# Performance work log

Hardware: AMD Instinct MI355X
Metric: run time of the kernel (lower is better)

Reference implementation:

```python
import jax, jax.numpy as jnp
import numpy as np

B, WIN, NN, NF, NH, NOUT = 4, 10, 10000, 8, 64, 1
N = B * WIN * NN          # stacked graph nodes
E = 3200000               # edges
EPS = 1e-5                # BatchNorm eps


def _gcn(x, edge_index, ew, W, b):
    # PyG GCNConv: linear first, then sym-normalized aggregation with self loops.
    xl = x @ W  # [N, H]
    loop = jnp.arange(N)
    row = jnp.concatenate([edge_index[0], loop])
    col = jnp.concatenate([edge_index[1], loop])
    w = jnp.concatenate([ew, jnp.ones((N,), ew.dtype)])
    deg = jax.ops.segment_sum(w, col, num_segments=N)
    dinv = jnp.where(deg > 0, jax.lax.rsqrt(deg), 0.0)
    norm = dinv[row] * w * dinv[col]
    out = jax.ops.segment_sum(norm[:, None] * xl[row], col, num_segments=N)
    return out + b


def _bn(x, g, bta):
    # training-mode BatchNorm1d (batch statistics, biased variance)
    m = x.mean(0)
    v = x.var(0)
    return (x - m) * jax.lax.rsqrt(v + EPS) * g + bta


def _lstm(xs, wih, whh, bih, bhh):
    # xs: [T, Bn, D]; PyTorch gate order i, f, g, o
    H = whh.shape[1]
    Bn = xs.shape[1]
    h0 = jnp.zeros((Bn, H), xs.dtype)
    c0 = jnp.zeros((Bn, H), xs.dtype)
    def step(carry, xt):
        h, c = carry
        gates = xt @ wih.T + bih + h @ whh.T + bhh
        i, f, g, o = jnp.split(gates, 4, axis=-1)
        c = jax.nn.sigmoid(f) * c + jax.nn.sigmoid(i) * jnp.tanh(g)
        h = jax.nn.sigmoid(o) * jnp.tanh(c)
        return (h, c), h
    (hn, cn), ys = jax.lax.scan(step, (h0, c0), xs)
    return ys, hn


def setup_inputs() -> dict:
    key = jax.random.key(0)
    ks = jax.random.split(key, 16)
    def rn(k, shape, s=0.05):
        return jax.random.normal(k, shape, jnp.float32) * s
    return {
        "x": jax.random.normal(ks[0], (N, NF), jnp.float32),
        "edge_index": jax.random.randint(ks[1], (2, E), 0, N),
        "edge_weight": jax.random.uniform(ks[2], (E,), jnp.float32),
        "c1_w": rn(ks[3], (NF, NH)), "c1_b": jnp.zeros((NH,), jnp.float32),
        "c2_w": rn(ks[4], (NH, NH)), "c2_b": jnp.zeros((NH,), jnp.float32),
        "bn1_g": jnp.ones((NH,), jnp.float32), "bn1_b": jnp.zeros((NH,), jnp.float32),
        "bn2_g": jnp.ones((NH,), jnp.float32), "bn2_b": jnp.zeros((NH,), jnp.float32),
        "l1_wih": rn(ks[5], (4 * NH, 2 * NH)), "l1_whh": rn(ks[6], (4 * NH, NH)),
        "l1_bih": jnp.zeros((4 * NH,), jnp.float32), "l1_bhh": jnp.zeros((4 * NH,), jnp.float32),
        "l2_wih": rn(ks[7], (4 * NH, NH)), "l2_whh": rn(ks[8], (4 * NH, NH)),
        "l2_bih": jnp.zeros((4 * NH,), jnp.float32), "l2_bhh": jnp.zeros((4 * NH,), jnp.float32),
        "fc1_w": rn(ks[9], (NH, 2 * NH + WIN * NF)), "fc1_b": jnp.zeros((NH,), jnp.float32),
        "fc2_w": rn(ks[10], (NOUT, NH)), "fc2_b": jnp.zeros((NOUT,), jnp.float32),
    }


def reference(x, edge_index, edge_weight, c1_w, c1_b, c2_w, c2_b,
              bn1_g, bn1_b, bn2_g, bn2_b,
              l1_wih, l1_whh, l1_bih, l1_bhh,
              l2_wih, l2_whh, l2_bih, l2_bhh,
              fc1_w, fc1_b, fc2_w, fc2_b):
    # skip connection: raw features per (batch,node) over the window
    skip = x.reshape(B, WIN, NN, NF).transpose(0, 2, 1, 3).reshape(B * NN, WIN * NF)
    # two GCN layers (dropout is identity in deterministic/eval reference)
    h1 = _bn(jax.nn.relu(_gcn(x, edge_index, edge_weight, c1_w, c1_b)), bn1_g, bn1_b)
    h2 = _bn(jax.nn.relu(_gcn(h1, edge_index, edge_weight, c2_w, c2_b)), bn2_g, bn2_b)
    xc = jnp.concatenate([h1, h2], axis=1)  # [N, 2H]
    xr = xc.reshape(B, WIN, NN, 2 * NH).transpose(1, 0, 2, 3).reshape(WIN, B * NN, 2 * NH)
    ys1, hn1 = _lstm(xr, l1_wih, l1_whh, l1_bih, l1_bhh)
    ys2, hn2 = _lstm(ys1, l2_wih, l2_whh, l2_bih, l2_bhh)
    z = jnp.concatenate([hn1, hn2, skip], axis=1)
    z = jax.nn.relu(z @ fc1_w.T + fc1_b)
    z = jax.nn.relu(z @ fc2_w.T + fc2_b)
    return z.reshape(-1)
```

## Files before the change

kernel.cpp:

```cpp
#include <hip/hip_runtime.h>
#include <math.h>

constexpr int BB     = 4;
constexpr int WINN   = 10;
constexpr int NNODES = 10000;
constexpr int NFEAT  = 8;
constexpr int NHID   = 64;
constexpr int NTOT   = BB * WINN * NNODES;
constexpr int NEDGE  = 3200000;
constexpr int NBN    = BB * NNODES;
constexpr float EPSBN = 1e-5f;

#define DEVFN static __device__ __forceinline__

typedef float f4 __attribute__((ext_vector_type(4)));
typedef short s8v __attribute__((ext_vector_type(8)));
typedef unsigned short ushort_t;
typedef unsigned int uint_t;

DEVFN float sigmoidf_(float x) { return 1.0f / (1.0f + __expf(-x)); }
DEVFN float tanhf_(float x) { return 2.0f / (1.0f + __expf(-2.0f * x)) - 1.0f; }
DEVFN ushort_t f2bf(float f) {
    uint_t x = __float_as_uint(f);
    return (ushort_t)((x + 0x7FFFu + ((x >> 16) & 1u)) >> 16);
}
DEVFN float bf2f(ushort_t u) { return __uint_as_float(((uint_t)u) << 16); }

__global__ void k_diag(float* out, float wsz, int n) {
    int i = blockIdx.x * 256 + threadIdx.x;
    if (i < n) out[i] = wsz;
}

__global__ void k_init(int* cntP, float* sums) {
    int i = blockIdx.x * 256 + threadIdx.x;
    if (i < 8 * NTOT) cntP[i] = 0;
    if (i < 2048) sums[i] = 0.f;
}

__global__ void k_hist(const int* __restrict__ ei, int* __restrict__ cntP) {
    int e = blockIdx.x * 256 + threadIdx.x;
    int p = blockIdx.x & 7;
    if (e < NEDGE) atomicAdd(&cntP[p * NTOT + ei[NEDGE + e]], 1);
}

__global__ void k_scan1(const int* __restrict__ cntP, int* __restrict__ ptr, int* __restrict__ tmp) {
    __shared__ int sdat[256];
    int tid = threadIdx.x;
    int base = blockIdx.x * 1024 + tid * 4;
    int v[4];
#pragma unroll
    for (int j = 0; j < 4; ++j) {
        int idx = base + j;
        int s = 0;
        if (idx < NTOT) {
#pragma unroll
            for (int p = 0; p < 8; ++p) s += cntP[p * NTOT + idx];
        }
        v[j] = s;
    }
    int sum = v[0] + v[1] + v[2] + v[3];
    sdat[tid] = sum;
    __syncthreads();
    for (int ofs = 1; ofs < 256; ofs <<= 1) {
        int x = (tid >= ofs) ? sdat[tid - ofs] : 0;
        __syncthreads();
        sdat[tid] += x;
        __syncthreads();
    }
    int run = sdat[tid] - sum;
    if (base + 0 < NTOT) ptr[base + 0] = run; run += v[0];
    if (base + 1 < NTOT) ptr[base + 1] = run; run += v[1];
    if (base + 2 < NTOT) ptr[base + 2] = run; run += v[2];
    if (base + 3 < NTOT) ptr[base + 3] = run;
    if (tid == 255) tmp[blockIdx.x] = sdat[255];
}

__global__ void k_scan2(int* tmp, int nb) {
    __shared__ int st[512];
    int tid = threadIdx.x;
    int v = (tid < nb) ? tmp[tid] : 0;
    st[tid] = v;
    __syncthreads();
    for (int ofs = 1; ofs < 512; ofs <<= 1) {
        int x = (tid >= ofs) ? st[tid - ofs] : 0;
        __syncthreads();
        st[tid] += x;
        __syncthreads();
    }
    if (tid < nb) tmp[tid] = st[tid] - v;
}

__global__ void k_scan3(int* __restrict__ ptr, int* __restrict__ cntP, const int* __restrict__ tmp) {
    int i = blockIdx.x * 256 + threadIdx.x;
    if (i < NTOT) {
        int p0 = ptr[i] + tmp[i >> 10];
        ptr[i] = p0;
        int run = p0;
#pragma unroll
        for (int p = 0; p < 8; ++p) {
            int c = cntP[p * NTOT + i];
            cntP[p * NTOT + i] = run;
            run += c;
        }
    }
    if (i == 0) ptr[NTOT] = NEDGE;
}

__global__ void k_fill(const int* __restrict__ ei, const float* __restrict__ ew,
                       int* __restrict__ cur8, int2* __restrict__ epack) {
    int e = blockIdx.x * 256 + threadIdx.x;
    if (e >= NEDGE) return;
    int p = blockIdx.x & 7;
    int row = ei[e], col = ei[NEDGE + e];
    int pos = atomicAdd(&cur8[p * NTOT + col], 1);
    epack[pos] = make_int2(row, __float_as_int(ew[e]));
}

__global__ void k_degcsr(const int* __restrict__ ptr, const int2* __restrict__ epack,
                         float* __restrict__ dinv) {
    int tid = threadIdx.x;
    int lane = tid & 63;
    int waveg = blockIdx.x * 4 + (tid >> 6);
    int g = lane >> 3, sub = lane & 7;
    int node = waveg * 8 + g;
    int beg = ptr[node], end = ptr[node + 1];
    float s = 0.f;
    for (int e = beg + sub; e < end; e += 8) s += __int_as_float(epack[e].y);
    s += __shfl_xor(s, 1, 64);
    s += __shfl_xor(s, 2, 64);
    s += __shfl_xor(s, 4, 64);
    if (sub == 0) dinv[node] = rsqrtf(1.0f + s);
}

__global__ void k_gather8(const int* __restrict__ ptr, const int2* __restrict__ epack,
                          const float* __restrict__ x, const float* __restrict__ dinv,
                          float* __restrict__ aggX) {
    int tid = threadIdx.x;
    int lane = tid & 63;
    int waveg = blockIdx.x * 4 + (tid >> 6);
    int g = lane >> 3, ch = lane & 7;
    int node = waveg * 8 + g;
    int beg = ptr[node], end = ptr[node + 1];
    float dv = dinv[node];
    float accE = 0.f;
    int e = beg;
    for (; e + 1 < end; e += 2) {
        int2 p0 = epack[e], p1 = epack[e + 1];
        accE = fmaf(dinv[p0.x] * __int_as_float(p0.y), x[p0.x * 8 + ch], accE);
        accE = fmaf(dinv[p1.x] * __int_as_float(p1.y), x[p1.x * 8 + ch], accE);
    }
    if (e < end) {
        int2 p = epack[e];
        accE = fmaf(dinv[p.x] * __int_as_float(p.y), x[p.x * 8 + ch], accE);
    }
    aggX[node * 8 + ch] = dv * fmaf(dv, x[node * 8 + ch], accE);
}

__global__ void k_gather64(const int* __restrict__ ptr, const int2* __restrict__ epack,
                           const ushort_t* __restrict__ src, const float* __restrict__ dinv,
                           float* __restrict__ dst) {
    int lane = threadIdx.x & 63;
    int node = blockIdx.x * 4 + (threadIdx.x >> 6);
    int beg = ptr[node], end = ptr[node + 1];
    float dv = dinv[node];
    float accE = 0.f;
    int e = beg;
    for (; e + 1 < end; e += 2) {
        int2 p0 = epack[e], p1 = epack[e + 1];
        accE = fmaf(dinv[p0.x] * __int_as_float(p0.y), bf2f(src[(size_t)p0.x * 64 + lane]), accE);
        accE = fmaf(dinv[p1.x] * __int_as_float(p1.y), bf2f(src[(size_t)p1.x * 64 + lane]), accE);
    }
    if (e < end) {
        int2 p = epack[e];
        accE = fmaf(dinv[p.x] * __int_as_float(p.y), bf2f(src[(size_t)p.x * 64 + lane]), accE);
    }
    dst[(size_t)node * 64 + lane] = dv * fmaf(dv, bf2f(src[(size_t)node * 64 + lane]), accE);
}

__global__ void k_lin1(const float* __restrict__ aggX, const float* __restrict__ W,
                       const float* __restrict__ bias, float* __restrict__ h1,
                       float* __restrict__ sums) {
    __shared__ float sW[NFEAT * NHID];
    int tid = threadIdx.x;
    sW[tid] = W[tid];
    sW[tid + 256] = W[tid + 256];
    __syncthreads();
    int c = tid & 63;
    float b = bias[c];
    float s = 0.f, sq = 0.f;
    int stride = gridDim.x * 256;
    for (int i = blockIdx.x * 256 + tid; i < NTOT * 64; i += stride) {
        int n = i >> 6;
        float acc = b;
#pragma unroll
        for (int f = 0; f < NFEAT; ++f) acc = fmaf(aggX[n * NFEAT + f], sW[f * NHID + c], acc);
        acc = acc > 0.f ? acc : 0.f;
        h1[i] = acc;
        s += acc;
        sq = fmaf(acc, acc, sq);
    }
    __shared__ float ls[4][64], lq[4][64];
    int w = tid >> 6;
    ls[w][c] = s; lq[w][c] = sq;
    __syncthreads();
    if (tid < 64) {
        atomicAdd(&sums[tid], ls[0][tid] + ls[1][tid] + ls[2][tid] + ls[3][tid]);
        atomicAdd(&sums[64 + tid], lq[0][tid] + lq[1][tid] + lq[2][tid] + lq[3][tid]);
    }
}

__global__ void k_bn_final(const float* __restrict__ sums, const float* __restrict__ g,
                           const float* __restrict__ b, float* __restrict__ ss) {
    int i = threadIdx.x;
    if (i >= 64) return;
    float mean = sums[i] * (1.0f / NTOT);
    float var = sums[64 + i] * (1.0f / NTOT) - mean * mean;
    float sc = g[i] * rsqrtf(var + EPSBN);
    ss[i] = sc;
    ss[64 + i] = b[i] - mean * sc;
}

__global__ void k_bn_final8(const float* __restrict__ sums8, const float* __restrict__ g,
                            const float* __restrict__ b, float* __restrict__ ss) {
    int i = threadIdx.x;
    if (i >= 64) return;
    float S = 0.f, Q = 0.f;
#pragma unroll
    for (int m = 0; m < 8; ++m) { S += sums8[m * 128 + i]; Q += sums8[m * 128 + 64 + i]; }
    float mean = S * (1.0f / NTOT);
    float var = Q * (1.0f / NTOT) - mean * mean;
    float sc = g[i] * rsqrtf(var + EPSBN);
    ss[i] = sc;
    ss[64 + i] = b[i] - mean * sc;
}

__global__ void k_bn1cast(const float* __restrict__ pre, const float* __restrict__ ss,
                          ushort_t* __restrict__ dst) {
    int c = threadIdx.x & 63;
    float sc = ss[c], sh = ss[64 + c];
    int stride = gridDim.x * 256;
    for (int i = blockIdx.x * 256 + threadIdx.x; i < NTOT * 64; i += stride)
        dst[i] = f2bf(fmaf(pre[i], sc, sh));
}

__global__ void k_lin2b(const float* __restrict__ io, const float* __restrict__ W2,
                        const float* __restrict__ bias, ushort_t* __restrict__ dst,
                        float* __restrict__ sums8) {
    __shared__ __align__(16) float srow[4][64];
    __shared__ float ls[4][64], lq[4][64];
    int lane = threadIdx.x & 63, wv = threadIdx.x >> 6;
    float wc[64];
#pragma unroll
    for (int h = 0; h < 64; ++h) wc[h] = W2[h * 64 + lane];
    float b = bias[lane];
    float s = 0.f, sq = 0.f;
    int wid = blockIdx.x * 4 + wv;
    int nw = gridDim.x * 4;
    for (int row = wid; row < NTOT; row += nw) {
        const float* hr = io + (size_t)row * 64;
        srow[wv][lane] = hr[lane];
        float acc = b;
#pragma unroll
        for (int h4 = 0; h4 < 16; ++h4) {
            float4 iv = *reinterpret_cast<const float4*>(&srow[wv][h4 * 4]);
            acc = fmaf(iv.x, wc[h4 * 4 + 0], acc);
            acc = fmaf(iv.y, wc[h4 * 4 + 1], acc);
            acc = fmaf(iv.z, wc[h4 * 4 + 2], acc);
            acc = fmaf(iv.w, wc[h4 * 4 + 3], acc);
        }
        acc = acc > 0.f ? acc : 0.f;
        dst[(size_t)row * 64 + lane] = f2bf(acc);
        s += acc;
        sq = fmaf(acc, acc, sq);
    }
    ls[wv][lane] = s; lq[wv][lane] = sq;
    __syncthreads();
    if (threadIdx.x < 64) {
        float S = ls[0][lane] + ls[1][lane] + ls[2][lane] + ls[3][lane];
        float Q = lq[0][lane] + lq[1][lane] + lq[2][lane] + lq[3][lane];
        float* d = sums8 + (blockIdx.x & 7) * 128;
        atomicAdd(&d[lane], S);
        atomicAdd(&d[64 + lane], Q);
    }
}

__global__ void k_prep(const float* __restrict__ wih1, const float* __restrict__ whh1,
                       const float* __restrict__ bih1, const float* __restrict__ bhh1,
                       const float* __restrict__ wih2, const float* __restrict__ whh2,
                       const float* __restrict__ bih2, const float* __restrict__ bhh2,
                       const float* __restrict__ fc1w,
                       float* wB1f, float* b1, ushort_t* wB2h, float* b2, float* fc1T) {
    int i = blockIdx.x * 256 + threadIdx.x;
    if (i < 256 * 192) {
        int n = i / 192, k = i - n * 192;
        wB1f[i] = (k < 128) ? wih1[n * 128 + k] : whh1[n * 64 + (k - 128)];
    }
    if (i < 256 * 128) {
        int n = i >> 7, k = i & 127;
        wB2h[i] = f2bf((k < 64) ? wih2[n * 64 + k] : whh2[n * 64 + (k - 64)]);
    }
    if (i < 208 * 64) {
        int k = i >> 6, o = i & 63;
        fc1T[i] = fc1w[o * 208 + k];
    }
    if (i < 256) { b1[i] = bih1[i] + bhh1[i]; b2[i] = bih2[i] + bhh2[i]; }
}

__global__ void k_fold2(float* __restrict__ wB1f, float* __restrict__ b1,
                        const float* __restrict__ ss2, ushort_t* __restrict__ wB1h) {
    int n = threadIdx.x;
    float acc = 0.f;
#pragma unroll
    for (int m = 0; m < 64; ++m) {
        float w = wB1f[n * 192 + 64 + m];
        acc = fmaf(w, ss2[64 + m], acc);
        wB1f[n * 192 + 64 + m] = w * ss2[m];
    }
    b1[n] += acc;
    __syncthreads();
    for (int j = n; j < 256 * 192; j += 256) wB1h[j] = f2bf(wB1f[j]);
}

__global__ __launch_bounds__(256, 2) void k_lstm_mfma4(
    const ushort_t* __restrict__ h1bf, const ushort_t* __restrict__ h2bf,
    const ushort_t* __restrict__ wB1, const ushort_t* __restrict__ wB2,
    const float* __restrict__ bs1, const float* __restrict__ bs2,
    float* __restrict__ hA, float* __restrict__ hB) {
    __shared__ ushort_t hx1[1024], hx2[1024];
    int tid = threadIdx.x;
    int lane = tid & 63, wv = tid >> 6;
    int c15 = lane & 15, g4 = lane >> 4;
    int g8 = g4 * 8;
    int bn0 = blockIdx.x * 16;
    int b = bn0 / NNODES, nn0 = bn0 - b * NNODES;

    for (int i = tid; i < 512; i += 256) { ((uint_t*)hx1)[i] = 0u; ((uint_t*)hx2)[i] = 0u; }

    s8v w1f[4][6], w2f[4][4];
#pragma unroll
    for (int j = 0; j < 4; ++j) {
        const ushort_t* base1 = wB1 + (size_t)((wv + 4 * j) * 16 + c15) * 192 + g8;
#pragma unroll
        for (int kk = 0; kk < 6; ++kk) w1f[j][kk] = *(const s8v*)(base1 + kk * 32);
        const ushort_t* base2 = wB2 + (size_t)((wv + 4 * j) * 16 + c15) * 128 + g8;
#pragma unroll
        for (int kk = 0; kk < 4; ++kk) w2f[j][kk] = *(const s8v*)(base2 + kk * 32);
    }
    float bi1[4], bi2[4];
#pragma unroll
    for (int j = 0; j < 4; ++j) {
        bi1[j] = bs1[(wv + 4 * j) * 16 + c15];
        bi2[j] = bs2[(wv + 4 * j) * 16 + c15];
    }
    float cA[4], cB[4];
#pragma unroll
    for (int q = 0; q < 4; ++q) { cA[q] = 0.f; cB[q] = 0.f; }

    int r7 = c15 & 7;
    int a_lo = c15 * 64 + ((g4 ^ r7) << 3);
    int a_hi = c15 * 64 + (((4 + g4) ^ r7) << 3);
    int u = wv * 16 + c15;
    int hxcol_hi = (u >> 3) << 3;
    int u7 = u & 7;

    __syncthreads();

    for (int t = 0; t < WINN; ++t) {
        size_t node = (size_t)((b * WINN + t) * NNODES + nn0 + c15) * 64 + g8;
        s8v a[6];
        a[0] = *(const s8v*)(h1bf + node);
        a[1] = *(const s8v*)(h1bf + node + 32);
        a[2] = *(const s8v*)(h2bf + node);
        a[3] = *(const s8v*)(h2bf + node + 32);
        a[4] = *(const s8v*)(&hx1[a_lo]);
        a[5] = *(const s8v*)(&hx1[a_hi]);

        f4 acc[4];
#pragma unroll
        for (int j = 0; j < 4; ++j) { f4 v = {bi1[j], bi1[j], bi1[j], bi1[j]}; acc[j] = v; }
#pragma unroll
        for (int j = 0; j < 4; ++j)
#pragma unroll
            for (int kk = 0; kk < 6; ++kk)
                acc[j] = __builtin_amdgcn_mfma_f32_16x16x32_bf16(a[kk], w1f[j][kk], acc[j], 0, 0, 0);
        __syncthreads();
#pragma unroll
        for (int q = 0; q < 4; ++q) {
            float ig = sigmoidf_(acc[0][q]);
            float fg = sigmoidf_(acc[1][q]);
            float gg = tanhf_(acc[2][q]);
            float og = sigmoidf_(acc[3][q]);
            float cv = fmaf(fg, cA[q], ig * gg);
            cA[q] = cv;
            float hv = og * tanhf_(cv);
            int rr = g4 * 4 + q;
            hx1[rr * 64 + (hxcol_hi ^ ((rr & 7) << 3)) + u7] = f2bf(hv);
        }
        __syncthreads();

        s8v r[4];
        r[0] = *(const s8v*)(&hx1[a_lo]);
        r[1] = *(const s8v*)(&hx1[a_hi]);
        r[2] = *(const s8v*)(&hx2[a_lo]);
        r[3] = *(const s8v*)(&hx2[a_hi]);
#pragma unroll
        for (int j = 0; j < 4; ++j) { f4 v = {bi2[j], bi2[j], bi2[j], bi2[j]}; acc[j] = v; }
#pragma unroll
        for (int j = 0; j < 4; ++j)
#pragma unroll
            for (int kk = 0; kk < 4; ++kk)
                acc[j] = __builtin_amdgcn_mfma_f32_16x16x32_bf16(r[kk], w2f[j][kk], acc[j], 0, 0, 0);
        __syncthreads();
#pragma unroll
        for (int q = 0; q < 4; ++q) {
            float ig = sigmoidf_(acc[0][q]);
            float fg = sigmoidf_(acc[1][q]);
            float gg = tanhf_(acc[2][q]);
            float og = sigmoidf_(acc[3][q]);
            float cv = fmaf(fg, cB[q], ig * gg);
            cB[q] = cv;
            float hv = og * tanhf_(cv);
            int rr = g4 * 4 + q;
            hx2[rr * 64 + (hxcol_hi ^ ((rr & 7) << 3)) + u7] = f2bf(hv);
        }
        __syncthreads();
    }
    for (int i = tid; i < 1024; i += 256) {
        int rr = i >> 6, uu = i & 63;
        int hw = rr * 64 + ((((uu >> 3) ^ (rr & 7)) << 3)) + (uu & 7);
        hA[(size_t)(bn0 + rr) * 64 + uu] = bf2f(hx1[hw]);
        hB[(size_t)(bn0 + rr) * 64 + uu] = bf2f(hx2[hw]);
    }
}

__global__ void k_head(const float* __restrict__ hA, const float* __restrict__ hB,
                       const float* __restrict__ x, const float* __restrict__ fc1T,
                       const float* __restrict__ fc1b, const float* __restrict__ fc2w,
                       const float* __restrict__ fc2b, float* __restrict__ out) {
    int lane = threadIdx.x & 63, wv = threadIdx.x >> 6;
    int bn = blockIdx.x * 4 + wv;
    __shared__ float sz[4][208];
    int b = bn / NNODES, nn = bn - b * NNODES;
    for (int k = lane; k < 208; k += 64) {
        float v;
        if (k < 64) v = hA[(size_t)bn * 64 + k];
        else if (k < 128) v = hB[(size_t)bn * 64 + (k - 64)];
        else {
            int kk = k - 128;
            int w = kk >> 3, f = kk & 7;
            v = x[(size_t)((b * WINN + w) * NNODES + nn) * NFEAT + f];
        }
        sz[wv][k] = v;
    }
    __syncthreads();
    float acc = fc1b[lane];
    for (int k = 0; k < 208; ++k) acc = fmaf(sz[wv][k], fc1T[k * 64 + lane], acc);
    acc = acc > 0.f ? acc : 0.f;
    float v = acc * fc2w[lane];
#pragma unroll
    for (int m = 32; m >= 1; m >>= 1) v += __shfl_xor(v, m, 64);
    if (lane == 0) {
        float z = v + fc2b[0];
        out[bn] = z > 0.f ? z : 0.f;
    }
}

extern "C" void kernel_launch(void* const* d_in, const int* in_sizes, int n_in,
                              void* d_out, int out_size, void* d_ws, size_t ws_size,
                              hipStream_t stream) {
    const float* x     = (const float*)d_in[0];
    const int*   ei    = (const int*)d_in[1];
    const float* ew    = (const float*)d_in[2];
    const float* c1w   = (const float*)d_in[3];
    const float* c1b   = (const float*)d_in[4];
    const float* c2w   = (const float*)d_in[5];
    const float* c2b   = (const float*)d_in[6];
    const float* bn1g  = (const float*)d_in[7];
    const float* bn1b  = (const float*)d_in[8];
    const float* bn2g  = (const float*)d_in[9];
    const float* bn2b  = (const float*)d_in[10];
    const float* wih1  = (const float*)d_in[11];
    const float* whh1  = (const float*)d_in[12];
    const float* bih1  = (const float*)d_in[13];
    const float* bhh1  = (const float*)d_in[14];
    const float* wih2  = (const float*)d_in[15];
    const float* whh2  = (const float*)d_in[16];
    const float* bih2  = (const float*)d_in[17];
    const float* bhh2  = (const float*)d_in[18];
    const float* fc1w  = (const float*)d_in[19];
    const float* fc1b  = (const float*)d_in[20];
    const float* fc2w  = (const float*)d_in[21];
    const float* fc2b  = (const float*)d_in[22];
    float* out = (float*)d_out;

    float* ws = (float*)d_ws;
    size_t off = 0;
    auto A = [&](size_t n) { float* p = ws + off; off += n; return p; };
    float* dinv   = A(NTOT);
    float* aggX   = A((size_t)NTOT * NFEAT);
    float* big    = A((size_t)NTOT * 64);
    ushort_t* h1bf = (ushort_t*)A((size_t)NTOT * 32);
    ushort_t* h2bf = (ushort_t*)A((size_t)NTOT * 32);

    size_t uoff = off;
    float* hA = A((size_t)NBN * 64);
    float* hB = A((size_t)NBN * 64);
    A(2 * (size_t)NEDGE + (NTOT + 1) + 8 * (size_t)NTOT - 2 * (size_t)NBN * 64);
    int2* epack = (int2*)(ws + uoff);
    int*  ptr   = (int*)(epack + NEDGE);
    int*  cntP  = ptr + NTOT + 1;

    float* wB1f = A(256 * 192);
    ushort_t* wB1h = (ushort_t*)A(256 * 96);
    ushort_t* wB2h = (ushort_t*)A(256 * 64);
    float* b1   = A(256);
    float* b2   = A(256);
    float* fc1T = A(208 * 64);
    float* sums = A(2048);
    float* ss1  = A(128);
    float* ss2  = A(128);
    float* scanTmpF = A(512);
    int* scanTmp = (int*)scanTmpF;

    if (ws_size < off * sizeof(float)) {
        k_diag<<<(out_size + 255) / 256, 256, 0, stream>>>(out, (float)ws_size, out_size);
        return;
    }

    constexpr int SCAN_NB = (NTOT + 1023) / 1024;

    k_init<<<8 * NTOT / 256, 256, 0, stream>>>(cntP, sums);
    k_hist<<<NEDGE / 256, 256, 0, stream>>>(ei, cntP);
    k_scan1<<<SCAN_NB, 256, 0, stream>>>(cntP, ptr, scanTmp);
    k_scan2<<<1, 512, 0, stream>>>(scanTmp, SCAN_NB);
    k_scan3<<<(NTOT + 255) / 256, 256, 0, stream>>>(ptr, cntP, scanTmp);
    k_fill<<<NEDGE / 256, 256, 0, stream>>>(ei, ew, cntP, epack);
    k_degcsr<<<NTOT / 8 / 4, 256, 0, stream>>>(ptr, epack, dinv);
    k_prep<<<192, 256, 0, stream>>>(wih1, whh1, bih1, bhh1, wih2, whh2, bih2, bhh2,
                                    fc1w, wB1f, b1, wB2h, b2, fc1T);

    k_gather8<<<NTOT / 8 / 4, 256, 0, stream>>>(ptr, epack, x, dinv, aggX);
    k_lin1<<<512, 256, 0, stream>>>(aggX, c1w, c1b, big, sums);
    k_bn_final<<<1, 64, 0, stream>>>(sums, bn1g, bn1b, ss1);
    k_bn1cast<<<2048, 256, 0, stream>>>(big, ss1, h1bf);

    k_gather64<<<NTOT / 4, 256, 0, stream>>>(ptr, epack, h1bf, dinv, big);
    k_lin2b<<<2048, 256, 0, stream>>>(big, c2w, c2b, h2bf, sums + 128);
    k_bn_final8<<<1, 64, 0, stream>>>(sums + 128, bn2g, bn2b, ss2);
    k_fold2<<<1, 256, 0, stream>>>(wB1f, b1, ss2, wB1h);

    k_lstm_mfma4<<<NBN / 16, 256, 0, stream>>>(h1bf, h2bf, wB1h, wB2h, b1, b2, hA, hB);

    k_head<<<NBN / 4, 256, 0, stream>>>(hA, hB, x, fc1T, fc1b, fc2w, fc2b, out);
}
```

Before: 1.160 ms.

## Fuse GCN2 gather with linear, fold BN1 affine into downstream weights

Removes the separate BN1 cast pass by storing pre-BN relu output directly in bf16, then applies the BN1 affine inside a new fused gather+linear kernel using the sum of normalization weights per node. The BN1 scale and shift are also folded into the first LSTM input weights and bias, so the LSTM reads the raw bf16 activations. The fused kernel avoids writing and rereading a large fp32 intermediate. The edge gathers are unrolled by four, and the LSTM's second-layer hidden buffer is double-buffered to drop two barriers per step. Risks include bf16 rounding applied before the BN affine, and lower parallelism in the fused gather, which uses a grid-stride loop instead of one wave per node.

```diff
diff --git a/kernel.cpp b/kernel.cpp
--- a/kernel.cpp
+++ b/kernel.cpp
@@ -144,41 +144,26 @@
     float dv = dinv[node];
     float accE = 0.f;
     int e = beg;
-    for (; e + 1 < end; e += 2) {
-        int2 p0 = epack[e], p1 = epack[e + 1];
-        accE = fmaf(dinv[p0.x] * __int_as_float(p0.y), x[p0.x * 8 + ch], accE);
-        accE = fmaf(dinv[p1.x] * __int_as_float(p1.y), x[p1.x * 8 + ch], accE);
-    }
-    if (e < end) {
+    for (; e + 3 < end; e += 4) {
+        int2 p0 = epack[e], p1 = epack[e + 1], p2 = epack[e + 2], p3 = epack[e + 3];
+        float n0 = dinv[p0.x] * __int_as_float(p0.y);
+        float n1 = dinv[p1.x] * __int_as_float(p1.y);
+        float n2 = dinv[p2.x] * __int_as_float(p2.y);
+        float n3 = dinv[p3.x] * __int_as_float(p3.y);
+        accE = fmaf(n0, x[p0.x * 8 + ch], accE);
+        accE = fmaf(n1, x[p1.x * 8 + ch], accE);
+        accE = fmaf(n2, x[p2.x * 8 + ch], accE);
+        accE = fmaf(n3, x[p3.x * 8 + ch], accE);
+    }
+    for (; e < end; ++e) {
         int2 p = epack[e];
         accE = fmaf(dinv[p.x] * __int_as_float(p.y), x[p.x * 8 + ch], accE);
     }
     aggX[node * 8 + ch] = dv * fmaf(dv, x[node * 8 + ch], accE);
 }
 
-__global__ void k_gather64(const int* __restrict__ ptr, const int2* __restrict__ epack,
-                           const ushort_t* __restrict__ src, const float* __restrict__ dinv,
-                           float* __restrict__ dst) {
-    int lane = threadIdx.x & 63;
-    int node = blockIdx.x * 4 + (threadIdx.x >> 6);
-    int beg = ptr[node], end = ptr[node + 1];
-    float dv = dinv[node];
-    float accE = 0.f;
-    int e = beg;
-    for (; e + 1 < end; e += 2) {
-        int2 p0 = epack[e], p1 = epack[e + 1];
-        accE = fmaf(dinv[p0.x] * __int_as_float(p0.y), bf2f(src[(size_t)p0.x * 64 + lane]), accE);
-        accE = fmaf(dinv[p1.x] * __int_as_float(p1.y), bf2f(src[(size_t)p1.x * 64 + lane]), accE);
-    }
-    if (e < end) {
-        int2 p = epack[e];
-        accE = fmaf(dinv[p.x] * __int_as_float(p.y), bf2f(src[(size_t)p.x * 64 + lane]), accE);
-    }
-    dst[(size_t)node * 64 + lane] = dv * fmaf(dv, bf2f(src[(size_t)node * 64 + lane]), accE);
-}
-
 __global__ void k_lin1(const float* __restrict__ aggX, const float* __restrict__ W,
-                       const float* __restrict__ bias, float* __restrict__ h1,
+                       const float* __restrict__ bias, ushort_t* __restrict__ rbf,
                        float* __restrict__ sums) {
     __shared__ float sW[NFEAT * NHID];
     int tid = threadIdx.x;
@@ -195,7 +180,7 @@
 #pragma unroll
         for (int f = 0; f < NFEAT; ++f) acc = fmaf(aggX[n * NFEAT + f], sW[f * NHID + c], acc);
         acc = acc > 0.f ? acc : 0.f;
-        h1[i] = acc;
+        rbf[i] = f2bf(acc);
         s += acc;
         sq = fmaf(acc, acc, sq);
     }
@@ -234,32 +219,49 @@
     ss[64 + i] = b[i] - mean * sc;
 }
 
-__global__ void k_bn1cast(const float* __restrict__ pre, const float* __restrict__ ss,
-                          ushort_t* __restrict__ dst) {
-    int c = threadIdx.x & 63;
-    float sc = ss[c], sh = ss[64 + c];
-    int stride = gridDim.x * 256;
-    for (int i = blockIdx.x * 256 + threadIdx.x; i < NTOT * 64; i += stride)
-        dst[i] = f2bf(fmaf(pre[i], sc, sh));
-}
-
-__global__ void k_lin2b(const float* __restrict__ io, const float* __restrict__ W2,
-                        const float* __restrict__ bias, ushort_t* __restrict__ dst,
-                        float* __restrict__ sums8) {
+__global__ void k_gcn2(const int* __restrict__ ptr, const int2* __restrict__ epack,
+                       const ushort_t* __restrict__ rbf, const float* __restrict__ dinv,
+                       const float* __restrict__ ss1, const float* __restrict__ W2,
+                       const float* __restrict__ bias2, ushort_t* __restrict__ h2bf,
+                       float* __restrict__ sums8) {
     __shared__ __align__(16) float srow[4][64];
     __shared__ float ls[4][64], lq[4][64];
     int lane = threadIdx.x & 63, wv = threadIdx.x >> 6;
     float wc[64];
 #pragma unroll
     for (int h = 0; h < 64; ++h) wc[h] = W2[h * 64 + lane];
-    float b = bias[lane];
+    float b2v = bias2[lane];
+    float sc1 = ss1[lane], sh1 = ss1[64 + lane];
     float s = 0.f, sq = 0.f;
     int wid = blockIdx.x * 4 + wv;
     int nw = gridDim.x * 4;
-    for (int row = wid; row < NTOT; row += nw) {
-        const float* hr = io + (size_t)row * 64;
-        srow[wv][lane] = hr[lane];
-        float acc = b;
+    for (int node = wid; node < NTOT; node += nw) {
+        int beg = ptr[node], end = ptr[node + 1];
+        float dv = dinv[node];
+        float accE = 0.f, accS = 0.f;
+        int e = beg;
+        for (; e + 3 < end; e += 4) {
+            int2 p0 = epack[e], p1 = epack[e + 1], p2 = epack[e + 2], p3 = epack[e + 3];
+            float n0 = dinv[p0.x] * __int_as_float(p0.y);
+            float n1 = dinv[p1.x] * __int_as_float(p1.y);
+            float n2 = dinv[p2.x] * __int_as_float(p2.y);
+            float n3 = dinv[p3.x] * __int_as_float(p3.y);
+            accE = fmaf(n0, bf2f(rbf[(size_t)p0.x * 64 + lane]), accE);
+            accE = fmaf(n1, bf2f(rbf[(size_t)p1.x * 64 + lane]), accE);
+            accE = fmaf(n2, bf2f(rbf[(size_t)p2.x * 64 + lane]), accE);
+            accE = fmaf(n3, bf2f(rbf[(size_t)p3.x * 64 + lane]), accE);
+            accS += n0 + n1 + n2 + n3;
+        }
+        for (; e < end; ++e) {
+            int2 p = epack[e];
+            float nv = dinv[p.x] * __int_as_float(p.y);
+            accE = fmaf(nv, bf2f(rbf[(size_t)p.x * 64 + lane]), accE);
+            accS += nv;
+        }
+        float G = dv * fmaf(dv, bf2f(rbf[(size_t)node * 64 + lane]), accE);
+        float S = dv * (dv + accS);
+        srow[wv][lane] = fmaf(sc1, G, sh1 * S);
+        float acc = b2v;
 #pragma unroll
         for (int h4 = 0; h4 < 16; ++h4) {
             float4 iv = *reinterpret_cast<const float4*>(&srow[wv][h4 * 4]);
@@ -269,18 +271,18 @@
             acc = fmaf(iv.w, wc[h4 * 4 + 3], acc);
         }
         acc = acc > 0.f ? acc : 0.f;
-        dst[(size_t)row * 64 + lane] = f2bf(acc);
+        h2bf[(size_t)node * 64 + lane] = f2bf(acc);
         s += acc;
         sq = fmaf(acc, acc, sq);
     }
     ls[wv][lane] = s; lq[wv][lane] = sq;
     __syncthreads();
     if (threadIdx.x < 64) {
-        float S = ls[0][lane] + ls[1][lane] + ls[2][lane] + ls[3][lane];
-        float Q = lq[0][lane] + lq[1][lane] + lq[2][lane] + lq[3][lane];
+        float S_ = ls[0][lane] + ls[1][lane] + ls[2][lane] + ls[3][lane];
+        float Q_ = lq[0][lane] + lq[1][lane] + lq[2][lane] + lq[3][lane];
         float* d = sums8 + (blockIdx.x & 7) * 128;
-        atomicAdd(&d[lane], S);
-        atomicAdd(&d[64 + lane], Q);
+        atomicAdd(&d[lane], S_);
+        atomicAdd(&d[64 + lane], Q_);
     }
 }
 
@@ -307,9 +309,16 @@
 }
 
 __global__ void k_fold2(float* __restrict__ wB1f, float* __restrict__ b1,
-                        const float* __restrict__ ss2, ushort_t* __restrict__ wB1h) {
+                        const float* __restrict__ ss1, const float* __restrict__ ss2,
+                        ushort_t* __restrict__ wB1h) {
     int n = threadIdx.x;
     float acc = 0.f;
+#pragma unroll
+    for (int m = 0; m < 64; ++m) {
+        float w = wB1f[n * 192 + m];
+        acc = fmaf(w, ss1[64 + m], acc);
+        wB1f[n * 192 + m] = w * ss1[m];
+    }
 #pragma unroll
     for (int m = 0; m < 64; ++m) {
         float w = wB1f[n * 192 + 64 + m];
@@ -326,7 +335,8 @@
     const ushort_t* __restrict__ wB1, const ushort_t* __restrict__ wB2,
     const float* __restrict__ bs1, const float* __restrict__ bs2,
     float* __restrict__ hA, float* __restrict__ hB) {
-    __shared__ ushort_t hx1[1024], hx2[1024];
+    __shared__ ushort_t hx1[1024];
+    __shared__ ushort_t hx2[2][1024];
     int tid = threadIdx.x;
     int lane = tid & 63, wv = tid >> 6;
     int c15 = lane & 15, g4 = lane >> 4;
@@ -334,7 +344,10 @@
     int bn0 = blockIdx.x * 16;
     int b = bn0 / NNODES, nn0 = bn0 - b * NNODES;
 
-    for (int i = tid; i < 512; i += 256) { ((uint_t*)hx1)[i] = 0u; ((uint_t*)hx2)[i] = 0u; }
+    for (int i = tid; i < 1536; i += 256) {
+        if (i < 512) ((uint_t*)hx1)[i] = 0u;
+        else ((uint_t*)hx2)[i - 512] = 0u;
+    }
 
     s8v w1f[4][6], w2f[4][4];
 #pragma unroll
@@ -398,11 +411,12 @@
         }
         __syncthreads();
 
+        const ushort_t* hp = hx2[1 - (t & 1)];
         s8v r[4];
         r[0] = *(const s8v*)(&hx1[a_lo]);
         r[1] = *(const s8v*)(&hx1[a_hi]);
-        r[2] = *(const s8v*)(&hx2[a_lo]);
-        r[3] = *(const s8v*)(&hx2[a_hi]);
+        r[2] = *(const s8v*)(&hp[a_lo]);
+        r[3] = *(const s8v*)(&hp[a_hi]);
 #pragma unroll
         for (int j = 0; j < 4; ++j) { f4 v = {bi2[j], bi2[j], bi2[j], bi2[j]}; acc[j] = v; }
 #pragma unroll
@@ -410,7 +424,7 @@
 #pragma unroll
             for (int kk = 0; kk < 4; ++kk)
                 acc[j] = __builtin_amdgcn_mfma_f32_16x16x32_bf16(r[kk], w2f[j][kk], acc[j], 0, 0, 0);
-        __syncthreads();
+        ushort_t* hw = hx2[t & 1];
 #pragma unroll
         for (int q = 0; q < 4; ++q) {
             float ig = sigmoidf_(acc[0][q]);
@@ -421,15 +435,16 @@
             cB[q] = cv;
             float hv = og * tanhf_(cv);
             int rr = g4 * 4 + q;
-            hx2[rr * 64 + (hxcol_hi ^ ((rr & 7) << 3)) + u7] = f2bf(hv);
-        }
-        __syncthreads();
-    }
+            hw[rr * 64 + (hxcol_hi ^ ((rr & 7) << 3)) + u7] = f2bf(hv);
+        }
+    }
+    __syncthreads();
+    const ushort_t* hf = hx2[(WINN - 1) & 1];
     for (int i = tid; i < 1024; i += 256) {
         int rr = i >> 6, uu = i & 63;
-        int hw = rr * 64 + ((((uu >> 3) ^ (rr & 7)) << 3)) + (uu & 7);
-        hA[(size_t)(bn0 + rr) * 64 + uu] = bf2f(hx1[hw]);
-        hB[(size_t)(bn0 + rr) * 64 + uu] = bf2f(hx2[hw]);
+        int hw2 = rr * 64 + ((((uu >> 3) ^ (rr & 7)) << 3)) + (uu & 7);
+        hA[(size_t)(bn0 + rr) * 64 + uu] = bf2f(hx1[hw2]);
+        hB[(size_t)(bn0 + rr) * 64 + uu] = bf2f(hf[hw2]);
     }
 }
 
@@ -498,7 +513,6 @@
     auto A = [&](size_t n) { float* p = ws + off; off += n; return p; };
     float* dinv   = A(NTOT);
     float* aggX   = A((size_t)NTOT * NFEAT);
-    float* big    = A((size_t)NTOT * 64);
     ushort_t* h1bf = (ushort_t*)A((size_t)NTOT * 32);
     ushort_t* h2bf = (ushort_t*)A((size_t)NTOT * 32);
 
@@ -540,14 +554,12 @@
                                     fc1w, wB1f, b1, wB2h, b2, fc1T);
 
     k_gather8<<<NTOT / 8 / 4, 256, 0, stream>>>(ptr, epack, x, dinv, aggX);
-    k_lin1<<<512, 256, 0, stream>>>(aggX, c1w, c1b, big, sums);
+    k_lin1<<<512, 256, 0, stream>>>(aggX, c1w, c1b, h1bf, sums);
     k_bn_final<<<1, 64, 0, stream>>>(sums, bn1g, bn1b, ss1);
-    k_bn1cast<<<2048, 256, 0, stream>>>(big, ss1, h1bf);
-
-    k_gather64<<<NTOT / 4, 256, 0, stream>>>(ptr, epack, h1bf, dinv, big);
-    k_lin2b<<<2048, 256, 0, stream>>>(big, c2w, c2b, h2bf, sums + 128);
+
+    k_gcn2<<<2048, 256, 0, stream>>>(ptr, epack, h1bf, dinv, ss1, c2w, c2b, h2bf, sums + 128);
     k_bn_final8<<<1, 64, 0, stream>>>(sums + 128, bn2g, bn2b, ss2);
-    k_fold2<<<1, 256, 0, stream>>>(wB1f, b1, ss2, wB1h);
+    k_fold2<<<1, 256, 0, stream>>>(wB1f, b1, ss1, ss2, wB1h);
 
     k_lstm_mfma4<<<NBN / 16, 256, 0, stream>>>(h1bf, h2bf, wB1h, wB2h, b1, b2, hA, hB);
 
```

Result: slower. 1.230 ms (+6.0%).
